# Performance work log

Hardware: AMD Instinct MI355X
Metric: run time of the kernel (lower is better)

Reference implementation:

```python
import jax, jax.numpy as jnp
import numpy as np
from functools import partial

THRESH = 0.5   # similarity_threshold
EPS = 1e-8     # F.cosine_similarity eps


def setup_inputs() -> dict:
    key = jax.random.key(0)
    # uniform positive vectors -> pairwise cosine ~0.75 > threshold, so merges actually occur
    embeddings = jax.random.uniform(key, (8192, 512), dtype=jnp.float32)
    return {"embeddings": embeddings}


@partial(jax.jit, static_argnums=())
def _greedy_match(embs):
    """One merge round. Returns (partner[i] or -1, consumed-as-j flag per i).
    Faithful to the original greedy: scan i in order; i picks argmax-sim j>i among
    not-yet-merged with sim >= threshold; both get marked merged."""
    n = embs.shape[0]
    norms = jnp.maximum(jnp.linalg.norm(embs, axis=-1), EPS)
    sim = (embs @ embs.T) / (norms[:, None] * norms[None, :])  # [n, n]
    idx = jnp.arange(n)

    def step(merged, xs):
        i, row = xs
        was_consumed = merged[i]
        valid = (~merged) & (idx > i)
        scores = jnp.where(valid, row, -jnp.inf)
        j = jnp.argmax(scores)
        ok = (~was_consumed) & (scores[j] >= THRESH)
        merged = merged.at[i].set(was_consumed | ok)
        merged = merged.at[j].set(merged[j] | ok)
        return merged, (jnp.where(ok, j, -1), was_consumed)

    _, (partners, consumed) = jax.lax.scan(step, jnp.zeros(n, bool), (idx, sim))
    return partners, consumed


def reference(embeddings):
    embs = embeddings
    # outer while-loop mirrors the module: iterate rounds until no merge or n<=1
    while embs.shape[0] > 1:
        partners, consumed = _greedy_match(embs)
        partners_np = np.asarray(partners)
        if not (partners_np >= 0).any():  # merge_occurred == False
            break
        safe = jnp.maximum(partners, 0)
        # fuse_embeddings: clamp(v1 + v2, max=1.0); non-leaders keep their row
        fused = jnp.where((partners >= 0)[:, None],
                          jnp.minimum(embs + embs[safe], 1.0), embs)
        survivors = np.where(~np.asarray(consumed))[0]  # rows not consumed as a j
        embs = fused[survivors]
    return embs
```

## Files before the change

kernel.cpp:

```cpp
#include <hip/hip_runtime.h>
#include <math.h>

#define D 512
#define THRESH 0.5f
#define NMAX 8192
#define TOPK 64
#define INFI 0x7fffffff

typedef short bhalf8 __attribute__((ext_vector_type(8)));
typedef float f32x4 __attribute__((ext_vector_type(4)));

__device__ __forceinline__ unsigned long long rdl64(unsigned long long x, int l) {
    unsigned lo = (unsigned)__builtin_amdgcn_readlane((int)(unsigned)(x & 0xffffffffull), l);
    unsigned hi = (unsigned)__builtin_amdgcn_readlane((int)(unsigned)(x >> 32), l);
    return ((unsigned long long)hi << 32) | lo;
}

__global__ void k_init(int* dn, int n) { *dn = n; }

__global__ void k_prep(const float* __restrict__ E, float* __restrict__ norms,
                       unsigned short* __restrict__ H, int* __restrict__ partner,
                       const int* __restrict__ dn) {
    int n = *dn;
    int row = blockIdx.x;
    if (row >= n) return;
    int t = threadIdx.x;
    float4 v = ((const float4*)(E + (size_t)row * D))[t];
    float s = v.x * v.x + v.y * v.y + v.z * v.z + v.w * v.w;
    #pragma unroll
    for (int o = 32; o > 0; o >>= 1) s += __shfl_down(s, o, 64);
    __shared__ float ls[2];
    if ((t & 63) == 0) ls[t >> 6] = s;
    float f[4] = {v.x, v.y, v.z, v.w};
    unsigned short r[4];
    #pragma unroll
    for (int u = 0; u < 4; ++u) {
        unsigned int b = __float_as_uint(f[u]);
        r[u] = (unsigned short)((b + 0x7FFFu + ((b >> 16) & 1u)) >> 16);
    }
    uint2 packed;
    packed.x = (unsigned)r[0] | ((unsigned)r[1] << 16);
    packed.y = (unsigned)r[2] | ((unsigned)r[3] << 16);
    *(uint2*)(H + (size_t)row * D + t * 4) = packed;
    if (t == 64) partner[row] = -1;
    __syncthreads();
    if (t == 0) norms[row] = fmaxf(sqrtf(ls[0] + ls[1]), 1e-8f);
}

#define LDSTRIDE 72
__global__ void __launch_bounds__(256) k_mfma_sim(
    const unsigned short* __restrict__ H, const float* __restrict__ norms,
    float* __restrict__ sim, int tile_start, int TR, int simStride,
    const int* __restrict__ dn)
{
    int n = *dn;
    if (tile_start >= n) return;
    int row0 = tile_start + blockIdx.y * 128;
    int col0 = blockIdx.x * 128;
    if (row0 >= n || col0 >= n) return;
    if (col0 + 128 <= row0 + 1) return;

    __shared__ unsigned short As[128 * LDSTRIDE];
    __shared__ unsigned short Bs[128 * LDSTRIDE];
    int tid = threadIdx.x;
    int lane = tid & 63;
    int wave = tid >> 6;
    int wr = wave >> 1;
    int wc = wave & 1;
    int krow = lane & 15;
    int kgrp = (lane >> 4) * 8;

    f32x4 acc[4][4];
    #pragma unroll
    for (int m = 0; m < 4; ++m)
        #pragma unroll
        for (int t = 0; t < 4; ++t)
            acc[m][t] = (f32x4){0.f, 0.f, 0.f, 0.f};

    for (int k0 = 0; k0 < D; k0 += 64) {
        #pragma unroll
        for (int it = 0; it < 4; ++it) {
            int c  = tid + it * 256;
            int rr = c >> 3;
            int cc = c & 7;
            uint4 va = make_uint4(0, 0, 0, 0);
            int gra = row0 + rr;
            if (gra < n) va = *(const uint4*)(H + (size_t)gra * D + k0 + cc * 8);
            *(uint4*)&As[rr * LDSTRIDE + cc * 8] = va;
            uint4 vb = make_uint4(0, 0, 0, 0);
            int grb = col0 + rr;
            if (grb < n) vb = *(const uint4*)(H + (size_t)grb * D + k0 + cc * 8);
            *(uint4*)&Bs[rr * LDSTRIDE + cc * 8] = vb;
        }
        __syncthreads();
        #pragma unroll
        for (int kk = 0; kk < 64; kk += 32) {
            bhalf8 a[4], b[4];
            #pragma unroll
            for (int m = 0; m < 4; ++m)
                a[m] = *(const bhalf8*)&As[(wr * 64 + m * 16 + krow) * LDSTRIDE + kk + kgrp];
            #pragma unroll
            for (int t = 0; t < 4; ++t)
                b[t] = *(const bhalf8*)&Bs[(wc * 64 + t * 16 + krow) * LDSTRIDE + kk + kgrp];
            #pragma unroll
            for (int m = 0; m < 4; ++m)
                #pragma unroll
                for (int t = 0; t < 4; ++t)
                    acc[m][t] = __builtin_amdgcn_mfma_f32_16x16x32_bf16(a[m], b[t], acc[m][t], 0, 0, 0);
        }
        __syncthreads();
    }

    int fcol = lane & 15;
    int frow = (lane >> 4) * 4;
    #pragma unroll
    for (int m = 0; m < 4; ++m) {
        #pragma unroll
        for (int t = 0; t < 4; ++t) {
            #pragma unroll
            for (int v = 0; v < 4; ++v) {
                int gr = row0 + wr * 64 + m * 16 + frow + v;
                int gc = col0 + wc * 64 + t * 16 + fcol;
                if (gr < n && gc < n)
                    sim[(size_t)(gr - tile_start) * simStride + gc] =
                        acc[m][t][v] / (norms[gr] * norms[gc]);
            }
        }
    }
}

__global__ void __launch_bounds__(64) k_topk(
    const float* __restrict__ sim, int tile_start, int TR, int simStride,
    uint2* __restrict__ tkP, int* __restrict__ needFix,
    const int* __restrict__ dn)
{
    int n = *dn;
    int r = blockIdx.x;
    int i = tile_start + r;
    if (r >= TR || i >= n) return;
    int lane = threadIdx.x;
    const float* srow = sim + (size_t)r * simStride;

    float v[8]; int id[8];
    #pragma unroll
    for (int u = 0; u < 8; ++u) { v[u] = -INFINITY; id[u] = INFI; }
    float ovV = -INFINITY; int ovI = INFI;

    for (int j = i + 1 + lane; j < n; j += 64) {
        float x = srow[j];
        if (x > v[7] || (x == v[7] && j < id[7])) {
            if (v[7] > ovV || (v[7] == ovV && id[7] < ovI)) { ovV = v[7]; ovI = id[7]; }
            int p = 7;
            #pragma unroll
            for (int u = 6; u >= 0; --u) {
                bool mv = (x > v[u]) || (x == v[u] && j < id[u]);
                if (mv) { v[u + 1] = v[u]; id[u + 1] = id[u]; p = u; }
            }
            v[p] = x; id[p] = j;
        } else {
            if (x > ovV || (x == ovV && j < ovI)) { ovV = x; ovI = j; }
        }
    }

    int pos = 0;
    float myV = -INFINITY; int myI = INFI;
    for (int k = 0; k < TOPK; ++k) {
        float hv = (pos < 8) ? v[pos] : -INFINITY;
        int   hi = (pos < 8) ? id[pos] : INFI;
        float bv = hv; int bi = hi;
        #pragma unroll
        for (int o = 1; o < 64; o <<= 1) {
            float xv = __shfl_xor(bv, o, 64);
            int   xi = __shfl_xor(bi, o, 64);
            if (xv > bv || (xv == bv && xi < bi)) { bv = xv; bi = xi; }
        }
        if (pos < 8 && hv == bv && hi == bi) pos++;
        if (k == lane) { myV = bv; myI = bi; }
    }
    tkP[(size_t)i * TOPK + lane] = make_uint2(__float_as_uint(myV), (unsigned)myI);

    float v64 = __shfl(myV, 63, 64);
    int   i64 = __shfl(myI, 63, 64);
    float oV = ovV; int oI = ovI;
    #pragma unroll
    for (int o = 1; o < 64; o <<= 1) {
        float xv = __shfl_xor(oV, o, 64);
        int   xi = __shfl_xor(oI, o, 64);
        if (xv > oV || (xv == oV && xi < oI)) { oV = xv; oI = xi; }
    }
    int bad = (oV > v64) || (oV == v64 && oI < i64);
    if (lane == 0) needFix[i] = bad;
}

__global__ void __launch_bounds__(64) k_topkfix(
    const float* __restrict__ sim, int tile_start, int TR, int simStride,
    uint2* __restrict__ tkP, const int* __restrict__ needFix,
    const int* __restrict__ dn)
{
    int n = *dn;
    int r = blockIdx.x;
    int i = tile_start + r;
    if (r >= TR || i >= n) return;
    if (!needFix[i]) return;
    int lane = threadIdx.x;
    __shared__ float lv[64][TOPK];
    __shared__ int   li[64][TOPK];
    for (int u = 0; u < TOPK; ++u) { lv[lane][u] = -INFINITY; li[lane][u] = INFI; }
    const float* srow = sim + (size_t)r * simStride;
    for (int j = i + 1 + lane; j < n; j += 64) {
        float x = srow[j];
        float wv = lv[lane][TOPK - 1]; int wi = li[lane][TOPK - 1];
        if (x > wv || (x == wv && j < wi)) {
            int p = TOPK - 1;
            for (int u = TOPK - 2; u >= 0; --u) {
                float uv = lv[lane][u]; int ui = li[lane][u];
                if (x > uv || (x == uv && j < ui)) { lv[lane][u + 1] = uv; li[lane][u + 1] = ui; p = u; }
                else break;
            }
            lv[lane][p] = x; li[lane][p] = j;
        }
    }
    int pos = 0;
    float myV = -INFINITY; int myI = INFI;
    for (int k = 0; k < TOPK; ++k) {
        float hv = (pos < TOPK) ? lv[lane][pos] : -INFINITY;
        int   hi = (pos < TOPK) ? li[lane][pos] : INFI;
        float bv = hv; int bi = hi;
        #pragma unroll
        for (int o = 1; o < 64; o <<= 1) {
            float xv = __shfl_xor(bv, o, 64);
            int   xi = __shfl_xor(bi, o, 64);
            if (xv > bv || (xv == bv && xi < bi)) { bv = xv; bi = xi; }
        }
        if (pos < TOPK && hv == bv && hi == bi) pos++;
        if (k == lane) { myV = bv; myI = bi; }
    }
    tkP[(size_t)i * TOPK + lane] = make_uint2(__float_as_uint(myV), (unsigned)myI);
}

__device__ __attribute__((noinline)) void sim_fallback(
    int r, int n, int lane, const float* __restrict__ sim, int simStride,
    const volatile unsigned long long* lmask, float& obv, int& obj)
{
    const float* srow = sim + (size_t)r * simStride;
    float bv = -INFINITY; int bj = INFI;
    for (int jb = (r + 1) & ~63; jb < n; jb += 64) {
        int j2 = jb + lane;
        unsigned long long wm = lmask[j2 >> 6];
        bool ok2 = (j2 > r) && (j2 < n) && !((wm >> (j2 & 63)) & 1ull);
        float v2 = ok2 ? srow[j2] : -INFINITY;
        int   i2 = ok2 ? j2 : INFI;
        if (v2 > bv || (v2 == bv && i2 < bj)) { bv = v2; bj = i2; }
    }
    #pragma unroll
    for (int o = 1; o < 64; o <<= 1) {
        float xv = __shfl_xor(bv, o, 64);
        int   xi = __shfl_xor(bj, o, 64);
        if (xv > bv || (xv == bv && xi < bj)) { bv = xv; bj = xi; }
    }
    obv = bv; obj = bj;
}

__device__ __attribute__((noinline)) void dot_fallback(
    int r, int n, int lane, const float* __restrict__ E,
    const float* __restrict__ norms, const volatile unsigned long long* lmask,
    float& obv, int& obj)
{
    float ni = norms[r];
    float4 e0 = *(const float4*)(E + (size_t)r * D + lane * 8);
    float4 e1 = *(const float4*)(E + (size_t)r * D + lane * 8 + 4);
    float bbv = -INFINITY; int bbj = INFI;
    int w0 = (r + 1) >> 6, wN = (n + 63) >> 6;
    for (int ww = w0; ww < wN; ++ww) {
        unsigned long long um = ~lmask[ww];
        if (ww == (r >> 6)) um &= (~0ull) << ((r & 63) + 1);
        int over = (ww << 6) + 64 - n;
        if (over > 0) um &= (over >= 64) ? 0ull : ((~0ull) >> over);
        while (um) {
            int b = __builtin_ctzll(um);
            um &= um - 1;
            int jj = (ww << 6) + b;
            float4 a0 = *(const float4*)(E + (size_t)jj * D + lane * 8);
            float4 a1 = *(const float4*)(E + (size_t)jj * D + lane * 8 + 4);
            float s = e0.x * a0.x + e0.y * a0.y + e0.z * a0.z + e0.w * a0.w
                    + e1.x * a1.x + e1.y * a1.y + e1.z * a1.z + e1.w * a1.w;
            #pragma unroll
            for (int o = 1; o < 64; o <<= 1) s += __shfl_xor(s, o, 64);
            float sv = s / (ni * norms[jj]);
            if (sv > bbv || (sv == bbv && jj < bbj)) { bbv = sv; bbj = jj; }
        }
    }
    obv = bbv; obj = bbj;
}

__global__ void __launch_bounds__(64) k_scan8(
    const uint2* __restrict__ tkP,
    const float* __restrict__ E, const float* __restrict__ norms,
    const float* __restrict__ sim, int simStride, int simOk,
    int* __restrict__ partner, int* __restrict__ srcIdx,
    int* __restrict__ dn)
{
    int n = *dn;
    int lane = threadIdx.x;
    int base_ = lane << 7;

    __shared__ unsigned long long lmask[128];
    lmask[lane] = 0ull;
    lmask[64 + lane] = 0ull;
    asm volatile("s_waitcnt lgkmcnt(0)" ::: "memory");

    unsigned long long own0 = 0ull, own1 = 0ull;
    unsigned long long cm0 = 0ull, cm1 = 0ull;
    int nextStart = 0;
    const uint2 SENT = make_uint2(0xFF800000u, (unsigned)INFI);

#define WINDOW(U0, U1, LO) {                                                   \
    long long kw_ = (long long)(LO) - base_;                                   \
    if (kw_ > 0) {                                                             \
        if (kw_ >= 128) { U0 = 0ull; U1 = 0ull; }                              \
        else if (kw_ >= 64) { U0 = 0ull; if (kw_ > 64) U1 &= (~0ull) << (int)(kw_ - 64); } \
        else U0 &= (~0ull) << (int)kw_;                                        \
    }                                                                          \
    int kn_ = n - base_;                                                       \
    if (kn_ <= 0) { U0 = 0ull; U1 = 0ull; }                                    \
    else if (kn_ < 64) { U0 &= (~0ull) >> (64 - kn_); U1 = 0ull; }             \
    else if (kn_ < 128) { U1 = (kn_ == 64) ? 0ull : (U1 & ((~0ull) >> (128 - kn_))); } }

#define ROWP(R0, R1, R2, R3, m) ((int)((((m) < 4 ? (R0) : (m) < 8 ? (R1) : (m) < 12 ? (R2) : (R3)) >> (((m) & 3) * 16)) & 0xffffull))

#define PUT16(R0, R1, R2, R3, g, v) {                                           \
    unsigned long long vv_ = ((unsigned long long)(unsigned)(v)) << (((g) & 3) * 16); \
    unsigned long long mm_ = 0xffffull << (((g) & 3) * 16);                     \
    if ((g) < 4) R0 = (R0 & ~mm_) | vv_;                                        \
    else if ((g) < 8) R1 = (R1 & ~mm_) | vv_;                                   \
    else if ((g) < 12) R2 = (R2 & ~mm_) | vv_;                                  \
    else R3 = (R3 & ~mm_) | vv_; }

#define BUILD16(R0, R1, R2, R3, CAND) do {                                      \
    R0 = ~0ull; R1 = ~0ull; R2 = ~0ull; R3 = ~0ull;                             \
    unsigned long long u0_ = ~own0, u1_ = ~own1;                                \
    WINDOW(u0_, u1_, nextStart)                                                 \
    unsigned long long balv_ = __ballot((u0_ | u1_) != 0ull);                   \
    int got_ = 0, lastSel_ = -1;                                                \
    while (got_ < 16 && balv_) {                                                \
        int L_ = (int)__builtin_ctzll(balv_); balv_ &= balv_ - 1;               \
        unsigned long long w0_ = rdl64(u0_, L_);                                \
        unsigned long long w1_ = rdl64(u1_, L_);                                \
        int bs_ = L_ << 7;                                                      \
        while (w0_ && got_ < 16) { int b_ = (int)__builtin_ctzll(w0_); w0_ &= w0_ - 1; \
            int v_ = bs_ + b_; PUT16(R0, R1, R2, R3, got_, v_); lastSel_ = v_; got_++; } \
        while (w1_ && got_ < 16) { int b_ = (int)__builtin_ctzll(w1_); w1_ &= w1_ - 1; \
            int v_ = bs_ + 64 + b_; PUT16(R0, R1, R2, R3, got_, v_); lastSel_ = v_; got_++; } \
    }                                                                           \
    nextStart = (got_ > 0) ? (lastSel_ + 1) : n;                                \
    _Pragma("unroll")                                                           \
    for (int m_ = 0; m_ < 16; ++m_) {                                           \
        int rm_ = ROWP(R0, R1, R2, R3, m_);                                     \
        CAND[m_] = (rm_ < n) ? tkP[(size_t)rm_ * TOPK + lane] : SENT;           \
    }                                                                           \
} while (0)

#define SETBIT(v) { if (lane == ((v) >> 7)) {                                   \
    if (((v) >> 6) & 1) { own1 |= 1ull << ((v) & 63); lmask[2*lane+1] = own1; } \
    else                { own0 |= 1ull << ((v) & 63); lmask[2*lane]   = own0; } } }
#define SETCMB(v) { if (lane == ((v) >> 7)) {                                   \
    if (((v) >> 6) & 1) cm1 |= 1ull << ((v) & 63);                              \
    else                cm0 |= 1ull << ((v) & 63); } }

    unsigned long long rpA0, rpA1, rpA2, rpA3, rpB0, rpB1, rpB2, rpB3;
    uint2 candA[16], candB[16];

    BUILD16(rpA0, rpA1, rpA2, rpA3, candA);
    int guard = NMAX + 8;
    while ((int)(rpA0 & 0xffffull) != 0xffff && guard-- > 0) {
        asm volatile("s_waitcnt lgkmcnt(0)" ::: "memory");
        unsigned act = 0;
        #pragma unroll
        for (int m = 0; m < 16; ++m) {
            int rm = ROWP(rpA0, rpA1, rpA2, rpA3, m);
            if (rm < n) {
                unsigned long long w = *(volatile unsigned long long*)&lmask[rm >> 6];
                if (!((w >> (rm & 63)) & 1ull)) act |= 1u << m;
            }
        }
        unsigned long long ball[16];
        #pragma unroll
        for (int m = 0; m < 16; ++m) {
            int ci = (int)candA[m].y;
            bool okc = ci < n;
            unsigned long long w = okc ? *(volatile unsigned long long*)&lmask[ci >> 6] : 0ull;
            bool valid = okc && !((w >> (ci & 63)) & 1ull);
            ball[m] = __ballot(valid);
        }
        BUILD16(rpB0, rpB1, rpB2, rpB3, candB);
        #pragma unroll
        for (int m = 0; m < 16; ++m) {
            if (!((act >> m) & 1u)) continue;
            int r_ = ROWP(rpA0, rpA1, rpA2, rpA3, m);
            unsigned long long b_ = ball[m];
            int j_ = -1; float v_ = -INFINITY;
            if (b_) {
                int L_ = (int)__builtin_ctzll(b_);
                j_ = __builtin_amdgcn_readlane((int)candA[m].y, L_);
                v_ = __uint_as_float((unsigned)__builtin_amdgcn_readlane((int)candA[m].x, L_));
            } else {
                unsigned long long u0_ = ~own0, u1_ = ~own1;
                WINDOW(u0_, u1_, r_ + 1)
                if (__ballot((u0_ | u1_) != 0ull)) {
                    asm volatile("s_waitcnt lgkmcnt(0)" ::: "memory");
                    if (simOk) sim_fallback(r_, n, lane, sim, simStride,
                                            (const volatile unsigned long long*)lmask, v_, j_);
                    else       dot_fallback(r_, n, lane, E, norms,
                                            (const volatile unsigned long long*)lmask, v_, j_);
                    if (j_ == INFI) j_ = -1;
                }
            }
            if (j_ >= 0 && v_ >= THRESH) {
                SETBIT(r_); SETBIT(j_); SETCMB(j_);
                if (lane == 0) partner[r_] = j_;
                #pragma unroll
                for (int m2 = 0; m2 < 16; ++m2) if (m2 > m) {
                    ball[m2] &= ~__ballot((int)candA[m2].y == j_);
                    if (ROWP(rpA0, rpA1, rpA2, rpA3, m2) == j_) act &= ~(1u << m2);
                }
            }
        }
        rpA0 = rpB0; rpA1 = rpB1; rpA2 = rpB2; rpA3 = rpB3;
        #pragma unroll
        for (int m = 0; m < 16; ++m) candA[m] = candB[m];
    }

    {
        int base = lane << 7;
        unsigned long long s0 = ~cm0, s1 = ~cm1;
        int kn = n - base;
        if (kn <= 0) { s0 = 0ull; s1 = 0ull; }
        else if (kn < 64) { s0 &= (~0ull) >> (64 - kn); s1 = 0ull; }
        else if (kn < 128) { s1 = (kn == 64) ? 0ull : (s1 & ((~0ull) >> (128 - kn))); }
        int cnt = __builtin_popcountll(s0) + __builtin_popcountll(s1);
        int inc = cnt;
        #pragma unroll
        for (int o = 1; o < 64; o <<= 1) {
            int t = __shfl_up(inc, o, 64);
            if (lane >= o) inc += t;
        }
        int p = inc - cnt;
        while (s0) { int b = __builtin_ctzll(s0); s0 &= s0 - 1; srcIdx[p++] = base + b; }
        while (s1) { int b = __builtin_ctzll(s1); s1 &= s1 - 1; srcIdx[p++] = base + 64 + b; }
        if (lane == 63) *dn = inc;
    }
#undef WINDOW
#undef ROWP
#undef PUT16
#undef BUILD16
#undef SETBIT
#undef SETCMB
}

__global__ void k_fuse(const float* __restrict__ cur, float* __restrict__ nxt,
                       const int* __restrict__ srcIdx, const int* __restrict__ partner,
                       const int* __restrict__ dn) {
    int nn = *dn;
    int k = blockIdx.x;
    if (k >= nn) return;
    int t = threadIdx.x;
    int i = srcIdx[k];
    int p = partner[i];
    float4 v = ((const float4*)(cur + (size_t)i * D))[t];
    if (p >= 0) {
        float4 w = ((const float4*)(cur + (size_t)p * D))[t];
        v.x = fminf(v.x + w.x, 1.0f);
        v.y = fminf(v.y + w.y, 1.0f);
        v.z = fminf(v.z + w.z, 1.0f);
        v.w = fminf(v.w + w.w, 1.0f);
    }
    ((float4*)(nxt + (size_t)k * D))[t] = v;
}

__global__ void k_copyout(const float* __restrict__ src, float* __restrict__ dst, int nelem) {
    int i = blockIdx.x * 256 + threadIdx.x;
    if (i < nelem) dst[i] = src[i];
}

extern "C" void kernel_launch(void* const* d_in, const int* in_sizes, int n_in,
                              void* d_out, int out_size, void* d_ws, size_t ws_size,
                              hipStream_t stream) {
    const float* input = (const float*)d_in[0];
    const int N0 = in_sizes[0] / D;
    char* ws = (char*)d_ws;

    const size_t embA = (size_t)(N0 / 2) * D * sizeof(float);
    const size_t embB = (size_t)(N0 / 4) * D * sizeof(float);
    const size_t embH = (size_t)N0 * D * sizeof(unsigned short);
    float* bufA = (float*)ws;
    float* bufB = (float*)(ws + embA);
    unsigned short* curh = (unsigned short*)(ws + embA + embB);
    char* aux = ws + embA + embB + embH;
    float* norms   = (float*)(aux);
    int*   partner = (int*)(aux + 32 * 1024);
    int*   srcIdx  = (int*)(aux + 96 * 1024);
    int*   dn      = (int*)(aux + 128 * 1024);
    int*   needFix = (int*)(aux + 160 * 1024);
    uint2* tkP     = (uint2*)(aux + 256 * 1024);
    float* simTile = (float*)(aux + 256 * 1024 + (size_t)NMAX * TOPK * 8);
    const size_t fixedBytes = embA + embB + embH + 256 * 1024 + (size_t)NMAX * TOPK * 8;

    int TR = NMAX;
    while (TR > 128 && fixedBytes + (size_t)TR * N0 * sizeof(float) > ws_size) TR >>= 1;
    int simOk = (TR == N0) ? 1 : 0;

    const int ROUNDS = 16;
    k_init<<<1, 1, 0, stream>>>(dn, N0);
    for (int r = 0; r < ROUNDS; ++r) {
        const float* cur = (r == 0) ? input : ((r & 1) ? bufA : bufB);
        float* nxt = (r & 1) ? bufB : bufA;
        k_prep<<<N0, 128, 0, stream>>>(cur, norms, curh, partner, dn);
        int NT = N0 / TR;
        for (int t = 0; t < NT; ++t) {
            dim3 g(N0 / 128, TR / 128);
            k_mfma_sim<<<g, 256, 0, stream>>>(curh, norms, simTile, t * TR, TR, N0, dn);
            k_topk<<<TR, 64, 0, stream>>>(simTile, t * TR, TR, N0, tkP, needFix, dn);
            k_topkfix<<<TR, 64, 0, stream>>>(simTile, t * TR, TR, N0, tkP, needFix, dn);
        }
        k_scan8<<<1, 64, 0, stream>>>(tkP, cur, norms, simTile, N0, simOk, partner, srcIdx, dn);
        k_fuse<<<N0, 128, 0, stream>>>(cur, nxt, srcIdx, partner, dn);
    }
    float* fin = bufB;
    k_copyout<<<(out_size + 255) / 256, 256, 0, stream>>>(fin, (float*)d_out, out_size);
}
```

Before: 15.61 ms.

## Restructure greedy scan to process 64-row windows with per-lane top-4 candidates

Replaces the 16-row software-pipelined greedy scan with a loop that picks the next 64 unmerged rows through a prefix sum over the ownership bitmasks. Each lane loads that row's top-4 candidates in two vector loads and marks which are still valid. Rows are then resolved serially through readlane, and when all four candidates are taken the code walks the rest of the top-K list before falling back to a full-row search. The aim is fewer serial iterations and less per-row candidate-building overhead. In exchange, volatile and waitcnt ordering on the shared mask is dropped, which is safe only because a single wavefront runs the scan, and deeper candidate misses cost more serial scalar work.

```diff
diff --git a/kernel.cpp b/kernel.cpp
--- a/kernel.cpp
+++ b/kernel.cpp
@@ -9,12 +9,6 @@
 
 typedef short bhalf8 __attribute__((ext_vector_type(8)));
 typedef float f32x4 __attribute__((ext_vector_type(4)));
-
-__device__ __forceinline__ unsigned long long rdl64(unsigned long long x, int l) {
-    unsigned lo = (unsigned)__builtin_amdgcn_readlane((int)(unsigned)(x & 0xffffffffull), l);
-    unsigned hi = (unsigned)__builtin_amdgcn_readlane((int)(unsigned)(x >> 32), l);
-    return ((unsigned long long)hi << 32) | lo;
-}
 
 __global__ void k_init(int* dn, int n) { *dn = n; }
 
@@ -240,7 +234,7 @@
 
 __device__ __attribute__((noinline)) void sim_fallback(
     int r, int n, int lane, const float* __restrict__ sim, int simStride,
-    const volatile unsigned long long* lmask, float& obv, int& obj)
+    const unsigned long long* lmask, float& obv, int& obj)
 {
     const float* srow = sim + (size_t)r * simStride;
     float bv = -INFINITY; int bj = INFI;
@@ -263,7 +257,7 @@
 
 __device__ __attribute__((noinline)) void dot_fallback(
     int r, int n, int lane, const float* __restrict__ E,
-    const float* __restrict__ norms, const volatile unsigned long long* lmask,
+    const float* __restrict__ norms, const unsigned long long* lmask,
     float& obv, int& obj)
 {
     float ni = norms[r];
@@ -293,7 +287,7 @@
     obv = bbv; obj = bbj;
 }
 
-__global__ void __launch_bounds__(64) k_scan8(
+__global__ void __launch_bounds__(64) k_scan9(
     const uint2* __restrict__ tkP,
     const float* __restrict__ E, const float* __restrict__ norms,
     const float* __restrict__ sim, int simStride, int simOk,
@@ -305,13 +299,12 @@
     int base_ = lane << 7;
 
     __shared__ unsigned long long lmask[128];
+    __shared__ int wslot[64];
     lmask[lane] = 0ull;
     lmask[64 + lane] = 0ull;
-    asm volatile("s_waitcnt lgkmcnt(0)" ::: "memory");
 
     unsigned long long own0 = 0ull, own1 = 0ull;
     unsigned long long cm0 = 0ull, cm1 = 0ull;
-    int nextStart = 0;
     const uint2 SENT = make_uint2(0xFF800000u, (unsigned)INFI);
 
 #define WINDOW(U0, U1, LO) {                                                   \
@@ -326,40 +319,6 @@
     else if (kn_ < 64) { U0 &= (~0ull) >> (64 - kn_); U1 = 0ull; }             \
     else if (kn_ < 128) { U1 = (kn_ == 64) ? 0ull : (U1 & ((~0ull) >> (128 - kn_))); } }
 
-#define ROWP(R0, R1, R2, R3, m) ((int)((((m) < 4 ? (R0) : (m) < 8 ? (R1) : (m) < 12 ? (R2) : (R3)) >> (((m) & 3) * 16)) & 0xffffull))
-
-#define PUT16(R0, R1, R2, R3, g, v) {                                           \
-    unsigned long long vv_ = ((unsigned long long)(unsigned)(v)) << (((g) & 3) * 16); \
-    unsigned long long mm_ = 0xffffull << (((g) & 3) * 16);                     \
-    if ((g) < 4) R0 = (R0 & ~mm_) | vv_;                                        \
-    else if ((g) < 8) R1 = (R1 & ~mm_) | vv_;                                   \
-    else if ((g) < 12) R2 = (R2 & ~mm_) | vv_;                                  \
-    else R3 = (R3 & ~mm_) | vv_; }
-
-#define BUILD16(R0, R1, R2, R3, CAND) do {                                      \
-    R0 = ~0ull; R1 = ~0ull; R2 = ~0ull; R3 = ~0ull;                             \
-    unsigned long long u0_ = ~own0, u1_ = ~own1;                                \
-    WINDOW(u0_, u1_, nextStart)                                                 \
-    unsigned long long balv_ = __ballot((u0_ | u1_) != 0ull);                   \
-    int got_ = 0, lastSel_ = -1;                                                \
-    while (got_ < 16 && balv_) {                                                \
-        int L_ = (int)__builtin_ctzll(balv_); balv_ &= balv_ - 1;               \
-        unsigned long long w0_ = rdl64(u0_, L_);                                \
-        unsigned long long w1_ = rdl64(u1_, L_);                                \
-        int bs_ = L_ << 7;                                                      \
-        while (w0_ && got_ < 16) { int b_ = (int)__builtin_ctzll(w0_); w0_ &= w0_ - 1; \
-            int v_ = bs_ + b_; PUT16(R0, R1, R2, R3, got_, v_); lastSel_ = v_; got_++; } \
-        while (w1_ && got_ < 16) { int b_ = (int)__builtin_ctzll(w1_); w1_ &= w1_ - 1; \
-            int v_ = bs_ + 64 + b_; PUT16(R0, R1, R2, R3, got_, v_); lastSel_ = v_; got_++; } \
-    }                                                                           \
-    nextStart = (got_ > 0) ? (lastSel_ + 1) : n;                                \
-    _Pragma("unroll")                                                           \
-    for (int m_ = 0; m_ < 16; ++m_) {                                           \
-        int rm_ = ROWP(R0, R1, R2, R3, m_);                                     \
-        CAND[m_] = (rm_ < n) ? tkP[(size_t)rm_ * TOPK + lane] : SENT;           \
-    }                                                                           \
-} while (0)
-
 #define SETBIT(v) { if (lane == ((v) >> 7)) {                                   \
     if (((v) >> 6) & 1) { own1 |= 1ull << ((v) & 63); lmask[2*lane+1] = own1; } \
     else                { own0 |= 1ull << ((v) & 63); lmask[2*lane]   = own0; } } }
@@ -367,67 +326,109 @@
     if (((v) >> 6) & 1) cm1 |= 1ull << ((v) & 63);                              \
     else                cm0 |= 1ull << ((v) & 63); } }
 
-    unsigned long long rpA0, rpA1, rpA2, rpA3, rpB0, rpB1, rpB2, rpB3;
-    uint2 candA[16], candB[16];
-
-    BUILD16(rpA0, rpA1, rpA2, rpA3, candA);
-    int guard = NMAX + 8;
-    while ((int)(rpA0 & 0xffffull) != 0xffff && guard-- > 0) {
-        asm volatile("s_waitcnt lgkmcnt(0)" ::: "memory");
-        unsigned act = 0;
-        #pragma unroll
-        for (int m = 0; m < 16; ++m) {
-            int rm = ROWP(rpA0, rpA1, rpA2, rpA3, m);
-            if (rm < n) {
-                unsigned long long w = *(volatile unsigned long long*)&lmask[rm >> 6];
-                if (!((w >> (rm & 63)) & 1ull)) act |= 1u << m;
-            }
-        }
-        unsigned long long ball[16];
-        #pragma unroll
-        for (int m = 0; m < 16; ++m) {
-            int ci = (int)candA[m].y;
-            bool okc = ci < n;
-            unsigned long long w = okc ? *(volatile unsigned long long*)&lmask[ci >> 6] : 0ull;
-            bool valid = okc && !((w >> (ci & 63)) & 1ull);
-            ball[m] = __ballot(valid);
-        }
-        BUILD16(rpB0, rpB1, rpB2, rpB3, candB);
-        #pragma unroll
-        for (int m = 0; m < 16; ++m) {
-            if (!((act >> m) & 1u)) continue;
-            int r_ = ROWP(rpA0, rpA1, rpA2, rpA3, m);
-            unsigned long long b_ = ball[m];
+    int cursor = 0;
+    int guardW = NMAX / 64 + 16;
+    while (cursor < n && guardW-- > 0) {
+        unsigned long long u0 = ~own0, u1 = ~own1;
+        WINDOW(u0, u1, cursor)
+        int myCnt = __builtin_popcountll(u0) + __builtin_popcountll(u1);
+        int incl = myCnt;
+        #pragma unroll
+        for (int o = 1; o < 64; o <<= 1) {
+            int t = __shfl_up(incl, o, 64);
+            if (lane >= o) incl += t;
+        }
+        int excl = incl - myCnt;
+        int total = __builtin_amdgcn_readlane(incl, 63);
+        if (total == 0) break;
+        if (excl < 64 && myCnt) {
+            int rk = excl;
+            unsigned long long t0 = u0;
+            while (t0 && rk < 64) { int b = __builtin_ctzll(t0); t0 &= t0 - 1; wslot[rk] = base_ + b; ++rk; }
+            unsigned long long t1 = u1;
+            while (t1 && rk < 64) { int b = __builtin_ctzll(t1); t1 &= t1 - 1; wslot[rk] = base_ + 64 + b; ++rk; }
+        }
+        int nw = (total < 64) ? total : 64;
+        int selR = (lane < nw) ? wslot[lane] : INFI;
+        cursor = (total > 64) ? (__builtin_amdgcn_readlane(selR, 63) + 1) : n;
+
+        uint2 c0 = SENT, c1 = SENT, c2 = SENT, c3 = SENT;
+        if (selR != INFI) {
+            const uint4* p = (const uint4*)(tkP + (size_t)selR * TOPK);
+            uint4 g0 = p[0];
+            uint4 g1 = p[1];
+            c0 = make_uint2(g0.x, g0.y); c1 = make_uint2(g0.z, g0.w);
+            c2 = make_uint2(g1.x, g1.y); c3 = make_uint2(g1.z, g1.w);
+        }
+        int i0 = (int)c0.y, i1 = (int)c1.y, i2 = (int)c2.y, i3 = (int)c3.y;
+        unsigned long long w0 = lmask[(i0 < n) ? (i0 >> 6) : 0];
+        unsigned long long w1 = lmask[(i1 < n) ? (i1 >> 6) : 0];
+        unsigned long long w2 = lmask[(i2 < n) ? (i2 >> 6) : 0];
+        unsigned long long w3 = lmask[(i3 < n) ? (i3 >> 6) : 0];
+        int vld = 0;
+        vld |= (i0 < n && !((w0 >> (i0 & 63)) & 1ull)) ? 1 : 0;
+        vld |= (i1 < n && !((w1 >> (i1 & 63)) & 1ull)) ? 2 : 0;
+        vld |= (i2 < n && !((w2 >> (i2 & 63)) & 1ull)) ? 4 : 0;
+        vld |= (i3 < n && !((w3 >> (i3 & 63)) & 1ull)) ? 8 : 0;
+
+        unsigned long long act = __ballot(selR != INFI);
+
+        while (act) {
+            int L_ = (int)__builtin_ctzll(act);
+            act &= act - 1;
+            int r_ = __builtin_amdgcn_readlane(selR, L_);
+            int vb = __builtin_amdgcn_readlane(vld, L_);
             int j_ = -1; float v_ = -INFINITY;
-            if (b_) {
-                int L_ = (int)__builtin_ctzll(b_);
-                j_ = __builtin_amdgcn_readlane((int)candA[m].y, L_);
-                v_ = __uint_as_float((unsigned)__builtin_amdgcn_readlane((int)candA[m].x, L_));
+            if (vb) {
+                int t_ = __builtin_ctz((unsigned)vb);
+                int jx, vx;
+                if (t_ == 0)      { jx = __builtin_amdgcn_readlane((int)c0.y, L_); vx = __builtin_amdgcn_readlane((int)c0.x, L_); }
+                else if (t_ == 1) { jx = __builtin_amdgcn_readlane((int)c1.y, L_); vx = __builtin_amdgcn_readlane((int)c1.x, L_); }
+                else if (t_ == 2) { jx = __builtin_amdgcn_readlane((int)c2.y, L_); vx = __builtin_amdgcn_readlane((int)c2.x, L_); }
+                else              { jx = __builtin_amdgcn_readlane((int)c3.y, L_); vx = __builtin_amdgcn_readlane((int)c3.x, L_); }
+                j_ = jx; v_ = __uint_as_float((unsigned)vx);
             } else {
-                unsigned long long u0_ = ~own0, u1_ = ~own1;
-                WINDOW(u0_, u1_, r_ + 1)
-                if (__ballot((u0_ | u1_) != 0ull)) {
-                    asm volatile("s_waitcnt lgkmcnt(0)" ::: "memory");
-                    if (simOk) sim_fallback(r_, n, lane, sim, simStride,
-                                            (const volatile unsigned long long*)lmask, v_, j_);
-                    else       dot_fallback(r_, n, lane, E, norms,
-                                            (const volatile unsigned long long*)lmask, v_, j_);
-                    if (j_ == INFI) j_ = -1;
+                unsigned long long s0 = ~own0, s1 = ~own1;
+                WINDOW(s0, s1, r_ + 1)
+                if (__ballot((s0 | s1) != 0ull)) {
+                    bool found = false;
+                    int bse = 4;
+                    while (!found && bse < TOPK) {
+                        uint2 q0 = tkP[(size_t)r_ * TOPK + bse + 0];
+                        uint2 q1 = tkP[(size_t)r_ * TOPK + bse + 1];
+                        uint2 q2 = tkP[(size_t)r_ * TOPK + bse + 2];
+                        uint2 q3 = tkP[(size_t)r_ * TOPK + bse + 3];
+                        #define TRYC(q) if (!found) { int ci = (int)q.y;        \
+                            if (ci < n) { unsigned long long wm = lmask[ci >> 6]; \
+                                if (!((wm >> (ci & 63)) & 1ull)) {              \
+                                    j_ = ci; v_ = __uint_as_float(q.x); found = true; } } }
+                        TRYC(q0) TRYC(q1) TRYC(q2) TRYC(q3)
+                        #undef TRYC
+                        bse += 4;
+                    }
+                    if (!found) {
+                        if (simOk) sim_fallback(r_, n, lane, sim, simStride,
+                                                (const unsigned long long*)lmask, v_, j_);
+                        else       dot_fallback(r_, n, lane, E, norms,
+                                                (const unsigned long long*)lmask, v_, j_);
+                        if (j_ == INFI) j_ = -1;
+                    }
                 }
             }
             if (j_ >= 0 && v_ >= THRESH) {
                 SETBIT(r_); SETBIT(j_); SETCMB(j_);
                 if (lane == 0) partner[r_] = j_;
-                #pragma unroll
-                for (int m2 = 0; m2 < 16; ++m2) if (m2 > m) {
-                    ball[m2] &= ~__ballot((int)candA[m2].y == j_);
-                    if (ROWP(rpA0, rpA1, rpA2, rpA3, m2) == j_) act &= ~(1u << m2);
-                }
+                act &= ~__ballot(selR == j_);
+                unsigned mm = 0;
+                mm |= ((int)c0.y == j_ || (int)c0.y == r_) ? 1u : 0u;
+                mm |= ((int)c1.y == j_ || (int)c1.y == r_) ? 2u : 0u;
+                mm |= ((int)c2.y == j_ || (int)c2.y == r_) ? 4u : 0u;
+                mm |= ((int)c3.y == j_ || (int)c3.y == r_) ? 8u : 0u;
+                vld &= ~(int)mm;
+            } else {
+                if (lane == 0) partner[r_] = -1;
             }
         }
-        rpA0 = rpB0; rpA1 = rpB1; rpA2 = rpB2; rpA3 = rpB3;
-        #pragma unroll
-        for (int m = 0; m < 16; ++m) candA[m] = candB[m];
     }
 
     {
@@ -450,9 +451,6 @@
         if (lane == 63) *dn = inc;
     }
 #undef WINDOW
-#undef ROWP
-#undef PUT16
-#undef BUILD16
 #undef SETBIT
 #undef SETCMB
 }
@@ -522,7 +520,7 @@
             k_topk<<<TR, 64, 0, stream>>>(simTile, t * TR, TR, N0, tkP, needFix, dn);
             k_topkfix<<<TR, 64, 0, stream>>>(simTile, t * TR, TR, N0, tkP, needFix, dn);
         }
-        k_scan8<<<1, 64, 0, stream>>>(tkP, cur, norms, simTile, N0, simOk, partner, srcIdx, dn);
+        k_scan9<<<1, 64, 0, stream>>>(tkP, cur, norms, simTile, N0, simOk, partner, srcIdx, dn);
         k_fuse<<<N0, 128, 0, stream>>>(cur, nxt, srcIdx, partner, dn);
     }
     float* fin = bufB;
```

New measurement: 19.26 ms. 23.4% more time.
